# Kernel optimization log

Measured on AMD Instinct MI355X. Metric: run time of the kernel, lower is better.

Reference implementation:

```python
import jax, jax.numpy as jnp
import numpy as np

B, M, L, IN_C, MID_C, OUT_C = 1, 128, 256, 256, 32, 128


def setup_inputs() -> dict:
    key = jax.random.key(0)
    k_x, k_proj, k_final = jax.random.split(key, 3)
    return {
        "x1d": jax.random.normal(k_x, (B, M, L, IN_C), dtype=jnp.float32),
        "norm_w": jnp.ones((IN_C,), dtype=jnp.float32),
        "norm_b": jnp.zeros((IN_C,), dtype=jnp.float32),
        "proj_w": jax.random.normal(k_proj, (2 * MID_C, IN_C), dtype=jnp.float32) * 0.02,
        "proj_b": jnp.zeros((2 * MID_C,), dtype=jnp.float32),
        "final_w": jax.random.normal(k_final, (OUT_C, MID_C * MID_C), dtype=jnp.float32) * 0.02,
        "final_b": jnp.zeros((OUT_C,), dtype=jnp.float32),
    }


def reference(x1d, norm_w, norm_b, proj_w, proj_b, final_w, final_b):
    # LayerNorm over channel dim
    mu = jnp.mean(x1d, axis=-1, keepdims=True)
    var = jnp.mean(jnp.square(x1d - mu), axis=-1, keepdims=True)
    x = (x1d - mu) * jax.lax.rsqrt(var + 1e-5) * norm_w + norm_b

    mid_c = proj_w.shape[0] // 2
    # Linear -> (b, m, L, 2*mid_c); view (..., mid_c, 2); chunk & squeeze:
    # i = interleaved even channels, j = interleaved odd channels
    p = jnp.einsum('bmlc,dc->bmld', x, proj_w) + proj_b
    p = p.reshape(*p.shape[:-1], mid_c, 2)
    i, j = p[..., 0], p[..., 1]          # each (b, m, L, mid_c)

    m = x1d.shape[1]
    # Outer product mean over the MSA (m) dimension -> (b, L, L, mid_c, mid_c)
    x2d = jnp.einsum('bmix,bmjy->bijxy', i, j) / m

    b, li, lj = x2d.shape[0], x2d.shape[1], x2d.shape[2]
    flat = x2d.reshape(b, li, lj, mid_c * mid_c)
    out = jnp.einsum('bijf,of->bijo', flat, final_w) + final_b
    return out
```

## Files before the change

### kernel.cpp

```cpp
#include <hip/hip_runtime.h>
#include <hip/hip_bf16.h>

#define DEVINL __device__ __forceinline__

typedef float  f32x4_t  __attribute__((ext_vector_type(4)));
typedef float  f32x16_t __attribute__((ext_vector_type(16)));
typedef short  bf16x8_t __attribute__((ext_vector_type(8)));

#define MFMA16(a,b,c) __builtin_amdgcn_mfma_f32_16x16x32_bf16((a),(b),(c),0,0,0)
#define MFMA32(a,b,c) __builtin_amdgcn_mfma_f32_32x32x16_bf16((a),(b),(c),0,0,0)

DEVINL unsigned short f2bf(float f) {
  union { float f; unsigned u; } v; v.f = f;
  unsigned r = v.u + 0x7fffu + ((v.u >> 16) & 1u);
  return (unsigned short)(r >> 16);
}

DEVINL unsigned pk2bf(float lo, float hi) {
  union { __hip_bfloat162 h2; unsigned u; } v;
  v.h2 = __float22bfloat162_rn(make_float2(lo, hi));
  return v.u;
}


__global__ __launch_bounds__(256) void kA(const float* __restrict__ x,
                                          const float* __restrict__ nw,
                                          const float* __restrict__ nb,
                                          const float* __restrict__ pw,
                                          const float* __restrict__ pb,
                                          const float* __restrict__ fw,
                                          unsigned short* __restrict__ Wb,
                                          unsigned short* __restrict__ Ig,
                                          unsigned short* __restrict__ Jg) {
  if (blockIdx.x >= 1024) {
    int T = (blockIdx.x - 1024) * 256 + threadIdx.x;
    int o     = T >> 8;
    int kpos0 = (T & 255) * 4;
    int y  = kpos0 >> 5;
    int x0 = kpos0 & 31;
    const float* fo = fw + o * 1024 + y;
    ushort4 u;
    u.x = f2bf(fo[(x0 + 0) * 32]);
    u.y = f2bf(fo[(x0 + 1) * 32]);
    u.z = f2bf(fo[(x0 + 2) * 32]);
    u.w = f2bf(fo[(x0 + 3) * 32]);
    size_t off = (size_t)((o >> 5) * 64 + (kpos0 >> 4)) * 512 + (o & 31) * 16
               + ((kpos0 >> 3) & 1) * 8 + (kpos0 & 7);
    *(ushort4*)&Wb[off] = u;
    return;
  }
  __shared__ unsigned short xnl[32 * 264];
  __shared__ unsigned short pwl[64 * 264];
  __shared__ unsigned short ep[64 * 36];
  const int tid  = threadIdx.x;
  const int wv   = tid >> 6;
  const int lane = tid & 63;
  const int q    = lane >> 4;
  const int ln16 = lane & 15;
  const int l    = blockIdx.x & 255;
  const int m0   = (blockIdx.x >> 8) * 32;

  const float4* xs = (const float4*)x;
  float4 v[8];
#pragma unroll
  for (int i = 0; i < 8; i++) {
    int row = m0 + i * 4 + wv;
    v[i] = xs[row * 16384 + l * 64 + lane];
  }
  float4 nw4 = ((const float4*)nw)[lane];
  float4 nb4 = ((const float4*)nb)[lane];

#pragma unroll
  for (int i = 0; i < 8; i++) {
    float s  = v[i].x + v[i].y + v[i].z + v[i].w;
    float ss = v[i].x * v[i].x + v[i].y * v[i].y + v[i].z * v[i].z + v[i].w * v[i].w;
#pragma unroll
    for (int off = 32; off > 0; off >>= 1) {
      s  += __shfl_xor(s, off);
      ss += __shfl_xor(ss, off);
    }
    float mu  = s * (1.0f / 256.0f);
    float var = ss * (1.0f / 256.0f) - mu * mu;
    float rs  = rsqrtf(var + 1e-5f);
    ushort4 u;
    u.x = f2bf((v[i].x - mu) * rs * nw4.x + nb4.x);
    u.y = f2bf((v[i].y - mu) * rs * nw4.y + nb4.y);
    u.z = f2bf((v[i].z - mu) * rs * nw4.z + nb4.z);
    u.w = f2bf((v[i].w - mu) * rs * nw4.w + nb4.w);
    *(ushort4*)&xnl[(i * 4 + wv) * 264 + lane * 4] = u;
  }

  const float4* ps = (const float4*)pw;
#pragma unroll
  for (int i = 0; i < 16; i++) {
    float4 w4 = ps[i * 256 + tid];
    ushort4 u;
    u.x = f2bf(w4.x); u.y = f2bf(w4.y); u.z = f2bf(w4.z); u.w = f2bf(w4.w);
    *(ushort4*)&pwl[(i * 4 + wv) * 264 + lane * 4] = u;
  }
  __syncthreads();

  const int rt = wv & 1;
  const int db = (wv >> 1) * 32;
  f32x4_t acc[2] = {{0.f, 0.f, 0.f, 0.f}, {0.f, 0.f, 0.f, 0.f}};
#pragma unroll
  for (int kc = 0; kc < 8; kc++) {
    bf16x8_t a  = *(const bf16x8_t*)&xnl[(rt * 16 + ln16) * 264 + kc * 32 + q * 8];
    bf16x8_t b0 = *(const bf16x8_t*)&pwl[(db + ln16) * 264 + kc * 32 + q * 8];
    bf16x8_t b1 = *(const bf16x8_t*)&pwl[(db + 16 + ln16) * 264 + kc * 32 + q * 8];
    acc[0] = MFMA16(a, b0, acc[0]);
    acc[1] = MFMA16(a, b1, acc[1]);
  }

#pragma unroll
  for (int t2 = 0; t2 < 2; t2++) {
    int d = db + t2 * 16 + ln16;
    float bias  = pb[d];
    float scale = (d & 1) ? 1.0f : (1.0f / 128.0f);
#pragma unroll
    for (int r = 0; r < 4; r++) {
      int mloc = rt * 16 + q * 4 + r;
      ep[d * 36 + mloc] = f2bf((acc[t2][r] + bias) * scale);
    }
  }
  __syncthreads();

  const int h  = tid >> 3;
  const int m4 = tid & 7;
  const size_t off = (size_t)(l * 8 + (m0 >> 4) + (m4 >> 2)) * 512 + h * 16 + ((m4 >> 1) & 1) * 8 + (m4 & 1) * 4;
  ushort4 vi = *(const ushort4*)&ep[(2 * h) * 36 + m4 * 4];
  *(ushort4*)&Ig[off] = vi;
  ushort4 vj = *(const ushort4*)&ep[(2 * h + 1) * 36 + m4 * 4];
  *(ushort4*)&Jg[off] = vj;
}

__global__ __launch_bounds__(512, 2) void kB(const unsigned short* __restrict__ Ig,
                                             const unsigned short* __restrict__ Jg,
                                             const unsigned short* __restrict__ Wb,
                                             const float* __restrict__ fb,
                                             float* __restrict__ out) {
  extern __shared__ unsigned short fl[];
  constexpr int P = 1048;
  const int tid  = threadIdx.x;
  const int w    = tid >> 6;
  const int lane = tid & 63;
  const int ln32 = lane & 31;
  const int h    = lane >> 5;
  const int p    = blockIdx.x >> 4;
  const int t    = blockIdx.x & 15;

  bf16x8_t jb[2][8];
  const size_t jbase = (size_t)(t * 16 + 2 * w) * 4096 + ln32 * 16 + h * 8;
#pragma unroll
  for (int mc = 0; mc < 8; mc++) jb[0][mc] = *(const bf16x8_t*)&Jg[jbase + mc * 512];
#pragma unroll
  for (int mc = 0; mc < 8; mc++) jb[1][mc] = *(const bf16x8_t*)&Jg[jbase + 4096 + mc * 512];

#pragma unroll
  for (int s = 0; s < 2; s++) {
    const int jl = 2 * w + s;
#pragma unroll
    for (int ilp = 0; ilp < 2; ilp++) {
      bf16x8_t af[2][8];
#pragma unroll
      for (int u = 0; u < 2; u++)
#pragma unroll
        for (int mc = 0; mc < 8; mc++)
          af[u][mc] = *(const bf16x8_t*)&Ig[(size_t)((p * 4 + ilp * 2 + u) * 8 + mc) * 512 + ln32 * 16 + h * 8];
      f32x16_t c[2];
#pragma unroll
      for (int i = 0; i < 16; i++) { c[0][i] = 0.f; c[1][i] = 0.f; }
#pragma unroll
      for (int mc = 0; mc < 8; mc++) {
        c[0] = MFMA32(af[0][mc], jb[s][mc], c[0]);
        c[1] = MFMA32(af[1][mc], jb[s][mc], c[1]);
      }
#pragma unroll
      for (int u = 0; u < 2; u++) {
        unsigned short* fr = &fl[((ilp * 2 + u) * 16 + jl) * P];
#pragma unroll
        for (int g = 0; g < 4; g++) {
          int cp = (4 * ln32 + g) ^ (ln32 & 7);
          uint2 pv;
          pv.x = pk2bf(c[u][4 * g + 0], c[u][4 * g + 1]);
          pv.y = pk2bf(c[u][4 * g + 2], c[u][4 * g + 3]);
          *(uint2*)&fr[cp * 8 + h * 4] = pv;
        }
      }
    }
  }

  const int ot = w & 3;
  const int kh = w >> 2;
  const unsigned short* Wp = Wb + (size_t)(ot * 64 + kh * 32) * 512 + ln32 * 16 + h * 8;
  bf16x8_t bq[4];
  bq[0] = *(const bf16x8_t*)&Wp[0];
  bq[1] = *(const bf16x8_t*)&Wp[512];

  __syncthreads();

  bq[2] = *(const bf16x8_t*)&Wp[2 * 512];
  bq[3] = *(const bf16x8_t*)&Wp[3 * 512];

#define LDA(rt, kc) (*(const bf16x8_t*)&fl[((rt) * 32 + ln32) * P + \
    ((((kh * 32 + (kc)) * 2 + h) ^ (((kh * 32 + (kc)) >> 1) & 7)) * 8)])

  f32x16_t o2[2];
#pragma unroll
  for (int i = 0; i < 16; i++) { o2[0][i] = 0.f; o2[1][i] = 0.f; }

  bf16x8_t a0 = LDA(0, 0), a1 = LDA(1, 0);
#pragma unroll
  for (int kc = 0; kc < 32; kc++) {
    bf16x8_t ac0 = a0, ac1 = a1, bc = bq[kc & 3];
    if (kc < 31) { a0 = LDA(0, kc + 1); a1 = LDA(1, kc + 1); }
    if (kc < 28) bq[kc & 3] = *(const bf16x8_t*)&Wp[(kc + 4) * 512];
    o2[0] = MFMA32(ac0, bc, o2[0]);
    o2[1] = MFMA32(ac1, bc, o2[1]);
  }
#undef LDA

  __syncthreads();
  float* red = (float*)fl;
  if (kh == 1) {
#pragma unroll
    for (int rt = 0; rt < 2; rt++) {
      float* bb = red + (ot * 2 + rt) * 1024 + lane * 2;
#pragma unroll
      for (int k = 0; k < 8; k++)
        *(float2*)&bb[k * 128] = make_float2(o2[rt][2 * k], o2[rt][2 * k + 1]);
    }
  }
  __syncthreads();
  if (kh == 0) {
    const float bias = fb[ot * 32 + ln32];
    float* ob = out + ((size_t)(p * 4) * 256 + t * 16) * 128 + ot * 32 + ln32;
#pragma unroll
    for (int rt = 0; rt < 2; rt++) {
      const float* bb = red + (ot * 2 + rt) * 1024 + lane * 2;
#pragma unroll
      for (int k = 0; k < 8; k++) {
        float2 rv = *(const float2*)&bb[k * 128];
        int r0 = 2 * k, r1 = 2 * k + 1;
        int br0 = rt * 32 + (r0 & 3) + 8 * (r0 >> 2) + 4 * h;
        int br1 = rt * 32 + (r1 & 3) + 8 * (r1 >> 2) + 4 * h;
        ob[(br0 >> 4) * 32768 + (br0 & 15) * 128] = o2[rt][r0] + rv.x + bias;
        ob[(br1 >> 4) * 32768 + (br1 & 15) * 128] = o2[rt][r1] + rv.y + bias;
      }
    }
  }
}

extern "C" void kernel_launch(void* const* d_in, const int* in_sizes, int n_in,
                              void* d_out, int out_size, void* d_ws, size_t ws_size,
                              hipStream_t stream) {
  const float* x1d     = (const float*)d_in[0];
  const float* norm_w  = (const float*)d_in[1];
  const float* norm_b  = (const float*)d_in[2];
  const float* proj_w  = (const float*)d_in[3];
  const float* proj_b  = (const float*)d_in[4];
  const float* final_w = (const float*)d_in[5];
  const float* final_b = (const float*)d_in[6];
  float* outp          = (float*)d_out;

  unsigned short* Wb  = (unsigned short*)d_ws;
  unsigned short* Igp = Wb + 131072;
  unsigned short* Jgp = Igp + 1048576;

  const int kb_lds = 64 * 1048 * 2;
  hipFuncSetAttribute((const void*)kB, hipFuncAttributeMaxDynamicSharedMemorySize, kb_lds);

  kA<<<1152, 256, 0, stream>>>(x1d, norm_w, norm_b, proj_w, proj_b, final_w, Wb, Igp, Jgp);
  kB<<<1024, 512, kb_lds, stream>>>(Igp, Jgp, Wb, final_b, outp);
}
```

Measured before the change: 138.1 us.

## Halve kB tile to 2x16 pairs and drop split-K LDS reduction

The outer-product/final-GEMM kernel now processes 2 i-rows by 16 j-columns per block with 256 threads, instead of 4 by 16 with 512 threads. The grid doubles and the LDS footprint halves. Each wave now runs the whole 1024-wide K loop for its 32 output columns, using two alternating accumulators, so the split-K LDS reduction and its extra barriers go away. The cost is more global/L2 traffic: J tiles and the full final weight matrix are re-read by twice as many blocks, and each wave streams all of W instead of half.

```diff
diff --git a/kernel.cpp b/kernel.cpp
--- a/kernel.cpp
+++ b/kernel.cpp
@@ -134,7 +134,7 @@
   *(ushort4*)&Jg[off] = vj;
 }
 
-__global__ __launch_bounds__(512, 2) void kB(const unsigned short* __restrict__ Ig,
+__global__ __launch_bounds__(256, 2) void kB(const unsigned short* __restrict__ Ig,
                                              const unsigned short* __restrict__ Jg,
                                              const unsigned short* __restrict__ Wb,
                                              const float* __restrict__ fb,
@@ -149,105 +149,83 @@
   const int p    = blockIdx.x >> 4;
   const int t    = blockIdx.x & 15;
 
-  bf16x8_t jb[2][8];
-  const size_t jbase = (size_t)(t * 16 + 2 * w) * 4096 + ln32 * 16 + h * 8;
-#pragma unroll
-  for (int mc = 0; mc < 8; mc++) jb[0][mc] = *(const bf16x8_t*)&Jg[jbase + mc * 512];
-#pragma unroll
-  for (int mc = 0; mc < 8; mc++) jb[1][mc] = *(const bf16x8_t*)&Jg[jbase + 4096 + mc * 512];
-
-#pragma unroll
-  for (int s = 0; s < 2; s++) {
-    const int jl = 2 * w + s;
-#pragma unroll
-    for (int ilp = 0; ilp < 2; ilp++) {
-      bf16x8_t af[2][8];
-#pragma unroll
-      for (int u = 0; u < 2; u++)
-#pragma unroll
-        for (int mc = 0; mc < 8; mc++)
-          af[u][mc] = *(const bf16x8_t*)&Ig[(size_t)((p * 4 + ilp * 2 + u) * 8 + mc) * 512 + ln32 * 16 + h * 8];
-      f32x16_t c[2];
-#pragma unroll
-      for (int i = 0; i < 16; i++) { c[0][i] = 0.f; c[1][i] = 0.f; }
-#pragma unroll
-      for (int mc = 0; mc < 8; mc++) {
-        c[0] = MFMA32(af[0][mc], jb[s][mc], c[0]);
-        c[1] = MFMA32(af[1][mc], jb[s][mc], c[1]);
+  bf16x8_t af[2][8];
+#pragma unroll
+  for (int u = 0; u < 2; u++)
+#pragma unroll
+    for (int mc = 0; mc < 8; mc++)
+      af[u][mc] = *(const bf16x8_t*)&Ig[(size_t)((p * 2 + u) * 8 + mc) * 512 + ln32 * 16 + h * 8];
+
+#pragma unroll
+  for (int s = 0; s < 4; s++) {
+    const int jl = 4 * w + s;
+    const size_t jbase = (size_t)(t * 16 + jl) * 4096 + ln32 * 16 + h * 8;
+    bf16x8_t jb[8];
+#pragma unroll
+    for (int mc = 0; mc < 8; mc++) jb[mc] = *(const bf16x8_t*)&Jg[jbase + mc * 512];
+    f32x16_t c[2];
+#pragma unroll
+    for (int i = 0; i < 16; i++) { c[0][i] = 0.f; c[1][i] = 0.f; }
+#pragma unroll
+    for (int mc = 0; mc < 8; mc++) {
+      c[0] = MFMA32(af[0][mc], jb[mc], c[0]);
+      c[1] = MFMA32(af[1][mc], jb[mc], c[1]);
+    }
+#pragma unroll
+    for (int u = 0; u < 2; u++) {
+      unsigned short* fr = &fl[(u * 16 + jl) * P];
+#pragma unroll
+      for (int g = 0; g < 4; g++) {
+        int cp = (4 * ln32 + g) ^ (ln32 & 7);
+        uint2 pv;
+        pv.x = pk2bf(c[u][4 * g + 0], c[u][4 * g + 1]);
+        pv.y = pk2bf(c[u][4 * g + 2], c[u][4 * g + 3]);
+        *(uint2*)&fr[cp * 8 + h * 4] = pv;
       }
-#pragma unroll
-      for (int u = 0; u < 2; u++) {
-        unsigned short* fr = &fl[((ilp * 2 + u) * 16 + jl) * P];
-#pragma unroll
-        for (int g = 0; g < 4; g++) {
-          int cp = (4 * ln32 + g) ^ (ln32 & 7);
-          uint2 pv;
-          pv.x = pk2bf(c[u][4 * g + 0], c[u][4 * g + 1]);
-          pv.y = pk2bf(c[u][4 * g + 2], c[u][4 * g + 3]);
-          *(uint2*)&fr[cp * 8 + h * 4] = pv;
-        }
-      }
-    }
-  }
-
-  const int ot = w & 3;
-  const int kh = w >> 2;
-  const unsigned short* Wp = Wb + (size_t)(ot * 64 + kh * 32) * 512 + ln32 * 16 + h * 8;
-  bf16x8_t bq[4];
+    }
+  }
+
+  const int ot = w;
+  const unsigned short* Wp = Wb + (size_t)(ot * 64) * 512 + ln32 * 16 + h * 8;
+  bf16x8_t bq[8];
   bq[0] = *(const bf16x8_t*)&Wp[0];
   bq[1] = *(const bf16x8_t*)&Wp[512];
 
   __syncthreads();
 
-  bq[2] = *(const bf16x8_t*)&Wp[2 * 512];
-  bq[3] = *(const bf16x8_t*)&Wp[3 * 512];
-
-#define LDA(rt, kc) (*(const bf16x8_t*)&fl[((rt) * 32 + ln32) * P + \
-    ((((kh * 32 + (kc)) * 2 + h) ^ (((kh * 32 + (kc)) >> 1) & 7)) * 8)])
+#pragma unroll
+  for (int i = 2; i < 8; i++) bq[i] = *(const bf16x8_t*)&Wp[(size_t)i * 512];
+
+#define LDA(kc) (*(const bf16x8_t*)&fl[ln32 * P + \
+    (((((kc) * 2 + h)) ^ (((kc) >> 1) & 7)) * 8)])
 
   f32x16_t o2[2];
 #pragma unroll
   for (int i = 0; i < 16; i++) { o2[0][i] = 0.f; o2[1][i] = 0.f; }
 
-  bf16x8_t a0 = LDA(0, 0), a1 = LDA(1, 0);
-#pragma unroll
-  for (int kc = 0; kc < 32; kc++) {
-    bf16x8_t ac0 = a0, ac1 = a1, bc = bq[kc & 3];
-    if (kc < 31) { a0 = LDA(0, kc + 1); a1 = LDA(1, kc + 1); }
-    if (kc < 28) bq[kc & 3] = *(const bf16x8_t*)&Wp[(kc + 4) * 512];
-    o2[0] = MFMA32(ac0, bc, o2[0]);
-    o2[1] = MFMA32(ac1, bc, o2[1]);
+  bf16x8_t aq[4];
+  aq[0] = LDA(0); aq[1] = LDA(1); aq[2] = LDA(2); aq[3] = LDA(3);
+
+#pragma unroll
+  for (int kc = 0; kc < 64; kc += 2) {
+    bf16x8_t ac0 = aq[kc & 3],      ac1 = aq[(kc + 1) & 3];
+    bf16x8_t bc0 = bq[kc & 7],      bc1 = bq[(kc + 1) & 7];
+    if (kc < 60) { aq[kc & 3] = LDA(kc + 4); aq[(kc + 1) & 3] = LDA(kc + 5); }
+    if (kc < 56) {
+      bq[kc & 7]       = *(const bf16x8_t*)&Wp[(size_t)(kc + 8) * 512];
+      bq[(kc + 1) & 7] = *(const bf16x8_t*)&Wp[(size_t)(kc + 9) * 512];
+    }
+    o2[0] = MFMA32(ac0, bc0, o2[0]);
+    o2[1] = MFMA32(ac1, bc1, o2[1]);
   }
 #undef LDA
 
-  __syncthreads();
-  float* red = (float*)fl;
-  if (kh == 1) {
-#pragma unroll
-    for (int rt = 0; rt < 2; rt++) {
-      float* bb = red + (ot * 2 + rt) * 1024 + lane * 2;
-#pragma unroll
-      for (int k = 0; k < 8; k++)
-        *(float2*)&bb[k * 128] = make_float2(o2[rt][2 * k], o2[rt][2 * k + 1]);
-    }
-  }
-  __syncthreads();
-  if (kh == 0) {
-    const float bias = fb[ot * 32 + ln32];
-    float* ob = out + ((size_t)(p * 4) * 256 + t * 16) * 128 + ot * 32 + ln32;
-#pragma unroll
-    for (int rt = 0; rt < 2; rt++) {
-      const float* bb = red + (ot * 2 + rt) * 1024 + lane * 2;
-#pragma unroll
-      for (int k = 0; k < 8; k++) {
-        float2 rv = *(const float2*)&bb[k * 128];
-        int r0 = 2 * k, r1 = 2 * k + 1;
-        int br0 = rt * 32 + (r0 & 3) + 8 * (r0 >> 2) + 4 * h;
-        int br1 = rt * 32 + (r1 & 3) + 8 * (r1 >> 2) + 4 * h;
-        ob[(br0 >> 4) * 32768 + (br0 & 15) * 128] = o2[rt][r0] + rv.x + bias;
-        ob[(br1 >> 4) * 32768 + (br1 & 15) * 128] = o2[rt][r1] + rv.y + bias;
-      }
-    }
+  const float bias = fb[ot * 32 + ln32];
+  float* ob = out + ((size_t)(p * 2) * 256 + t * 16) * 128 + ot * 32 + ln32;
+#pragma unroll
+  for (int r = 0; r < 16; r++) {
+    int br = (r & 3) + 8 * (r >> 2) + 4 * h;
+    ob[(br >> 4) * 32768 + (br & 15) * 128] = o2[0][r] + o2[1][r] + bias;
   }
 }
 
@@ -267,9 +245,9 @@
   unsigned short* Igp = Wb + 131072;
   unsigned short* Jgp = Igp + 1048576;
 
-  const int kb_lds = 64 * 1048 * 2;
+  const int kb_lds = 32 * 1048 * 2;
   hipFuncSetAttribute((const void*)kB, hipFuncAttributeMaxDynamicSharedMemorySize, kb_lds);
 
   kA<<<1152, 256, 0, stream>>>(x1d, norm_w, norm_b, proj_w, proj_b, final_w, Wb, Igp, Jgp);
-  kB<<<1024, 512, kb_lds, stream>>>(Igp, Jgp, Wb, final_b, outp);
-}
+  kB<<<2048, 256, kb_lds, stream>>>(Igp, Jgp, Wb, final_b, outp);
+}
```

Measured after the change: 134.8 us. 1.02x faster.
